# Performance work log

Measured on AMD Instinct MI355X. Metric: run time of the kernel, lower is better.

## Reference

```python
import jax, jax.numpy as jnp
import numpy as np

N_NODES = 50000
N_EDGES = 1600000
D_IN = 512
D_HEAD = 64
N_HEADS_L1 = 4


def _segment_mean(data, seg_ids, num_segments, counts):
    s = jax.ops.segment_sum(data, seg_ids, num_segments=num_segments)
    denom = jnp.maximum(counts, 1.0)
    return jnp.where(counts[:, None] > 0, s / denom[:, None], 0.0)


def setup_inputs() -> dict:
    key = jax.random.key(0)
    k1, k2, k3, k4 = jax.random.split(key, 4)
    node_features = jax.random.normal(k1, (N_NODES, D_IN), dtype=jnp.float32)
    edge_index = jax.random.randint(k2, (2, N_EDGES), 0, N_NODES, dtype=jnp.int32)
    W1 = jax.random.normal(k3, (N_HEADS_L1, D_IN, D_HEAD), dtype=jnp.float32) * (1.0 / np.sqrt(D_IN))
    W2 = jax.random.normal(k4, (N_HEADS_L1 * D_HEAD, D_HEAD), dtype=jnp.float32) * (1.0 / np.sqrt(N_HEADS_L1 * D_HEAD))
    return {"node_features": node_features, "edge_index": edge_index, "W1": W1, "W2": W2}


def reference(node_features, edge_index, W1, W2):
    n = node_features.shape[0]
    src = edge_index[0]  # segment ids (destination of aggregation in TF code)
    dst = edge_index[1]  # gathered neighbors
    counts = jax.ops.segment_sum(jnp.ones_like(src, dtype=node_features.dtype), src, num_segments=n)

    # Layer 1: 4 heads, Dense(64, no bias) -> gather(dst) -> unsorted_segment_mean(src) -> concat -> elu
    head_outs = []
    for i in range(N_HEADS_L1):
        t = node_features @ W1[i]                 # (N, 64)
        agg = _segment_mean(t[dst], src, n, counts)  # (N, 64)
        head_outs.append(agg)
    h = jax.nn.elu(jnp.concatenate(head_outs, axis=-1))  # (N, 256)

    # Layer 2: 1 head, linear activation
    t2 = h @ W2                                   # (N, 64)
    out = _segment_mean(t2[dst], src, n, counts)  # (N, 64)
    return out
```

## Files before the change

### kernel.cpp

```cpp
#include <hip/hip_runtime.h>
#include <hip/hip_bf16.h>
#include <stdint.h>

#define N_NODES 50000
#define N_EDGES 1600000
#define D_IN    512
#define D_H1    256
#define D_OUT   64

#define NBUK    196
#define MAXB    9216
#define EPB     4096
#define NPB     391
#define SLOT    96

typedef __attribute__((ext_vector_type(8))) short  short8;
typedef __attribute__((ext_vector_type(4))) float  f32x4;
typedef __attribute__((ext_vector_type(4))) unsigned int u32x4;
typedef __attribute__((ext_vector_type(2))) unsigned int u32x2;

static __device__ __forceinline__ unsigned short f2bf(float f) {
    union { float f; unsigned int u; } c; c.f = f;
    unsigned int u = c.u;
    return (unsigned short)((u + 0x7FFFu + ((u >> 16) & 1u)) >> 16);
}
static __device__ __forceinline__ float bf2f(unsigned short b) {
    union { unsigned int u; float f; } c; c.u = ((unsigned int)b) << 16;
    return c.f;
}
static __device__ __forceinline__ float bflo(unsigned int v) { return bf2f((unsigned short)(v & 0xffffu)); }
static __device__ __forceinline__ float bfhi(unsigned int v) { return bf2f((unsigned short)(v >> 16)); }


__global__ __launch_bounds__(256) void part_kernel(const int* __restrict__ src,
                                                   const int* __restrict__ dst,
                                                   int* __restrict__ gcnt,
                                                   unsigned int* __restrict__ gbuk) {
    __shared__ int hist[NBUK];
    __shared__ int lofs[NBUK];
    __shared__ int gbase[NBUK];
    __shared__ int sbuf[256];
    __shared__ unsigned int sorted[EPB];
    __shared__ unsigned char bid[EPB];

    const int t  = threadIdx.x;
    const int e0 = blockIdx.x * EPB;
    int ec = N_EDGES - e0; if (ec > EPB) ec = EPB;

    for (int i = t; i < NBUK; i += 256) hist[i] = 0;
    __syncthreads();

    unsigned int rec[16];
    int bb[16], idx[16];
#pragma unroll
    for (int j = 0; j < 16; ++j) {
        int i = j * 256 + t;
        if (i < ec) {
            int s = src[e0 + i], d = dst[e0 + i];
            int b = s >> 8;
            rec[j] = ((unsigned int)(s & 255) << 16) | (unsigned int)d;
            bb[j]  = b;
            idx[j] = atomicAdd(&hist[b], 1);
        } else bb[j] = -1;
    }
    __syncthreads();

    int v = (t < NBUK) ? hist[t] : 0;
    sbuf[t] = v;
    __syncthreads();
#pragma unroll
    for (int off = 1; off < 256; off <<= 1) {
        int x = (t >= off) ? sbuf[t - off] : 0;
        __syncthreads();
        sbuf[t] += x;
        __syncthreads();
    }
    if (t < NBUK) {
        lofs[t]  = sbuf[t] - v;
        gbase[t] = atomicAdd(&gcnt[t], v);
    }
    __syncthreads();

#pragma unroll
    for (int j = 0; j < 16; ++j) {
        if (bb[j] >= 0) {
            int p = lofs[bb[j]] + idx[j];
            sorted[p] = rec[j];
            bid[p] = (unsigned char)bb[j];
        }
    }
    __syncthreads();

    for (int i = t; i < ec; i += 256) {
        int b = bid[i];
        int p = gbase[b] + (i - lofs[b]);
        gbuk[(size_t)b * MAXB + p] = sorted[i];
    }
}


__global__ __launch_bounds__(256) void sort_kernel(const int* __restrict__ gcnt,
                                                   const unsigned int* __restrict__ gbuk,
                                                   unsigned short* __restrict__ sdst,
                                                   int* __restrict__ deg) {
    __shared__ int hist[256];
    __shared__ int nofs[256];
    __shared__ int sbuf[256];
    __shared__ unsigned short list[MAXB];

    const int t = threadIdx.x;
    const int b = blockIdx.x;
    const int cnt = gcnt[b];
    const unsigned int* buk = gbuk + (size_t)b * MAXB;

    hist[t] = 0;
    __syncthreads();
    for (int i = t; i < cnt; i += 256)
        atomicAdd(&hist[buk[i] >> 16], 1);
    __syncthreads();

    int v = hist[t];
    sbuf[t] = v;
    __syncthreads();
#pragma unroll
    for (int off = 1; off < 256; off <<= 1) {
        int x = (t >= off) ? sbuf[t - off] : 0;
        __syncthreads();
        sbuf[t] += x;
        __syncthreads();
    }
    nofs[t] = sbuf[t] - v;
    const int n = b * 256 + t;
    if (n < N_NODES) deg[n] = v;
    __syncthreads();

    for (int i = t; i < cnt; i += 256) {
        unsigned int r = buk[i];
        int p = atomicAdd(&nofs[r >> 16], 1);
        list[p] = (unsigned short)(r & 0xffffu);
    }
    __syncthreads();

    if (n < N_NODES && v > 0) {
        int beg = nofs[t] - v;
        unsigned short* out = sdst + (size_t)n * SLOT;
        for (int j = 0; j < v; ++j) out[j] = list[beg + j];
    }
}


__global__ void convw_kernel(const float* __restrict__ W1, const float* __restrict__ W2,
                             unsigned short* __restrict__ Bt1, unsigned short* __restrict__ Bt2) {
    int i = blockIdx.x * 256 + threadIdx.x;
    if (i < 4 * 512 * 64) {
        int h = i >> 15;
        int k = (i >> 6) & 511;
        int j = i & 63;
        Bt1[(h * 64 + j) * 512 + k] = f2bf(W1[i]);
    } else {
        int r = i - 4 * 512 * 64;
        if (r < 256 * 64) {
            int k = r >> 6;
            int n = r & 63;
            Bt2[n * 256 + k] = f2bf(W2[r]);
        }
    }
}


__global__ __launch_bounds__(512) void gemm1_kernel(const float* __restrict__ A,
                                                    const unsigned short* __restrict__ Bt,
                                                    unsigned short* __restrict__ C) {
    constexpr int BM = 128, BN = 256, BK = 32, LDK = 40, K = D_IN, M = N_NODES, N = D_H1;
    __shared__ unsigned short As[BM * LDK];
    __shared__ unsigned short Bs[BN * LDK];

    const int tid  = threadIdx.x;
    const int lane = tid & 63;
    const int w    = tid >> 6;
    const int wm   = (w >> 2) * 64;
    const int wn   = (w & 3) * 64;
    const int quad = lane >> 4;
    const int l15  = lane & 15;
    const int bm   = blockIdx.x;

    f32x4 acc[4][4];
#pragma unroll
    for (int mi = 0; mi < 4; ++mi)
#pragma unroll
        for (int ni = 0; ni < 4; ++ni)
            acc[mi][ni] = (f32x4){0.f, 0.f, 0.f, 0.f};

    const int r0 = tid >> 2;
    const int f8 = tid & 3;

    for (int k0 = 0; k0 < K; k0 += BK) {
        {
            int grow = bm * BM + r0;
            if (grow >= M) grow = M - 1;
            const float* ap = A + (size_t)grow * K + k0 + f8 * 8;
            f32x4 v0 = *(const f32x4*)ap;
            f32x4 v1 = *(const f32x4*)(ap + 4);
            u32x4 pk;
            pk[0] = (unsigned int)f2bf(v0[0]) | ((unsigned int)f2bf(v0[1]) << 16);
            pk[1] = (unsigned int)f2bf(v0[2]) | ((unsigned int)f2bf(v0[3]) << 16);
            pk[2] = (unsigned int)f2bf(v1[0]) | ((unsigned int)f2bf(v1[1]) << 16);
            pk[3] = (unsigned int)f2bf(v1[2]) | ((unsigned int)f2bf(v1[3]) << 16);
            *(u32x4*)&As[r0 * LDK + f8 * 8] = pk;
        }
        {
#pragma unroll
            for (int p = 0; p < 2; ++p) {
                int row = p * 128 + r0;
                u32x4 v = *(const u32x4*)(Bt + (size_t)row * K + k0 + f8 * 8);
                *(u32x4*)&Bs[row * LDK + f8 * 8] = v;
            }
        }
        __syncthreads();

        short8 af[4], bfr[4];
#pragma unroll
        for (int mi = 0; mi < 4; ++mi)
            af[mi] = *(const short8*)&As[(wm + mi * 16 + l15) * LDK + quad * 8];
#pragma unroll
        for (int ni = 0; ni < 4; ++ni)
            bfr[ni] = *(const short8*)&Bs[(wn + ni * 16 + l15) * LDK + quad * 8];
#pragma unroll
        for (int mi = 0; mi < 4; ++mi)
#pragma unroll
            for (int ni = 0; ni < 4; ++ni)
                acc[mi][ni] = __builtin_amdgcn_mfma_f32_16x16x32_bf16(af[mi], bfr[ni], acc[mi][ni], 0, 0, 0);
        __syncthreads();
    }

#pragma unroll
    for (int mi = 0; mi < 4; ++mi) {
        int row0 = bm * BM + wm + mi * 16 + quad * 4;
#pragma unroll
        for (int ni = 0; ni < 4; ++ni) {
            int col = wn + ni * 16 + l15;
#pragma unroll
            for (int r = 0; r < 4; ++r) {
                int row = row0 + r;
                if (row < M) C[(size_t)row * N + col] = f2bf(acc[mi][ni][r]);
            }
        }
    }
}


__global__ __launch_bounds__(256) void gemm2_kernel(const unsigned short* __restrict__ A,
                                                    const unsigned short* __restrict__ Bt,
                                                    unsigned short* __restrict__ C) {
    constexpr int BM = 64, BN = 64, BK = 32, LDK = 40, K = D_H1, M = N_NODES, N = D_OUT;
    __shared__ unsigned short As[BM * LDK];
    __shared__ unsigned short Bs[BN * LDK];

    const int tid  = threadIdx.x;
    const int lane = tid & 63;
    const int w    = tid >> 6;
    const int wm   = (w >> 1) * 32;
    const int wn   = (w & 1) * 32;
    const int quad = lane >> 4;
    const int l15  = lane & 15;
    const int bm   = blockIdx.x;

    f32x4 acc[2][2];
#pragma unroll
    for (int mi = 0; mi < 2; ++mi)
#pragma unroll
        for (int ni = 0; ni < 2; ++ni)
            acc[mi][ni] = (f32x4){0.f, 0.f, 0.f, 0.f};

    for (int k0 = 0; k0 < K; k0 += BK) {
        {
            int f8 = tid & 3;
            int r0 = tid >> 2;
            int grow = bm * BM + r0;
            if (grow >= M) grow = M - 1;
            u32x4 v = *(const u32x4*)(A + (size_t)grow * K + k0 + f8 * 8);
            *(u32x4*)&As[r0 * LDK + f8 * 8] = v;
        }
        {
            int f8 = tid & 3;
            int r0 = tid >> 2;
            u32x4 v = *(const u32x4*)(Bt + (size_t)r0 * K + k0 + f8 * 8);
            *(u32x4*)&Bs[r0 * LDK + f8 * 8] = v;
        }
        __syncthreads();

        short8 af[2], bfr[2];
#pragma unroll
        for (int mi = 0; mi < 2; ++mi)
            af[mi] = *(const short8*)&As[(wm + mi * 16 + l15) * LDK + quad * 8];
#pragma unroll
        for (int ni = 0; ni < 2; ++ni)
            bfr[ni] = *(const short8*)&Bs[(wn + ni * 16 + l15) * LDK + quad * 8];
#pragma unroll
        for (int mi = 0; mi < 2; ++mi)
#pragma unroll
            for (int ni = 0; ni < 2; ++ni)
                acc[mi][ni] = __builtin_amdgcn_mfma_f32_16x16x32_bf16(af[mi], bfr[ni], acc[mi][ni], 0, 0, 0);
        __syncthreads();
    }

#pragma unroll
    for (int mi = 0; mi < 2; ++mi) {
        int row0 = bm * BM + wm + mi * 16 + quad * 4;
#pragma unroll
        for (int ni = 0; ni < 2; ++ni) {
            int col = wn + ni * 16 + l15;
#pragma unroll
            for (int r = 0; r < 4; ++r) {
                int row = row0 + r;
                if (row < M) C[(size_t)row * N + col] = f2bf(acc[mi][ni][r]);
            }
        }
    }
}


__global__ __launch_bounds__(256) void agg1_kernel(const unsigned short* __restrict__ t,
                                                   const int* __restrict__ deg,
                                                   const unsigned short* __restrict__ sdst,
                                                   unsigned short* __restrict__ h) {
    int s = __builtin_amdgcn_readfirstlane(blockIdx.x * 4 + (threadIdx.x >> 6));
    int lane = threadIdx.x & 63;
    int sub = lane >> 5;
    int c   = lane & 31;
    int end = deg[s];
    const unsigned short* el = sdst + (size_t)s * SLOT;
    const unsigned short* base = t + 8 * c;

    float a[8];
#pragma unroll
    for (int k = 0; k < 8; ++k) a[k] = 0.f;

    int e = 0;
    for (; e + 8 <= end; e += 8) {
        int i0 = el[e + 0 + sub], i1 = el[e + 2 + sub];
        int i2 = el[e + 4 + sub], i3 = el[e + 6 + sub];
        u32x4 v0 = *(const u32x4*)(base + (size_t)i0 * D_H1);
        u32x4 v1 = *(const u32x4*)(base + (size_t)i1 * D_H1);
        u32x4 v2 = *(const u32x4*)(base + (size_t)i2 * D_H1);
        u32x4 v3 = *(const u32x4*)(base + (size_t)i3 * D_H1);
#pragma unroll
        for (int q = 0; q < 4; ++q) {
            a[2 * q]     += (bflo(v0[q]) + bflo(v1[q])) + (bflo(v2[q]) + bflo(v3[q]));
            a[2 * q + 1] += (bfhi(v0[q]) + bfhi(v1[q])) + (bfhi(v2[q]) + bfhi(v3[q]));
        }
    }
    for (; e + 2 <= end; e += 2) {
        int i0 = el[e + sub];
        u32x4 v = *(const u32x4*)(base + (size_t)i0 * D_H1);
#pragma unroll
        for (int q = 0; q < 4; ++q) {
            a[2 * q]     += bflo(v[q]);
            a[2 * q + 1] += bfhi(v[q]);
        }
    }
    if (e < end && sub == 0) {
        int i0 = el[e];
        u32x4 v = *(const u32x4*)(base + (size_t)i0 * D_H1);
#pragma unroll
        for (int q = 0; q < 4; ++q) {
            a[2 * q]     += bflo(v[q]);
            a[2 * q + 1] += bfhi(v[q]);
        }
    }
#pragma unroll
    for (int k = 0; k < 8; ++k) a[k] += __shfl_xor(a[k], 32);

    if (sub == 0) {
        float iv = (end > 0) ? (1.0f / (float)end) : 0.f;
        u32x4 pk;
#pragma unroll
        for (int q = 0; q < 4; ++q) {
            float m0 = a[2 * q] * iv, m1 = a[2 * q + 1] * iv;
            m0 = (m0 > 0.f) ? m0 : (__expf(m0) - 1.f);
            m1 = (m1 > 0.f) ? m1 : (__expf(m1) - 1.f);
            pk[q] = (unsigned int)f2bf(m0) | ((unsigned int)f2bf(m1) << 16);
        }
        *(u32x4*)&h[(size_t)s * D_H1 + 8 * c] = pk;
    }
}

__global__ __launch_bounds__(256) void agg2_kernel(const unsigned short* __restrict__ t2,
                                                   const int* __restrict__ deg,
                                                   const unsigned short* __restrict__ sdst,
                                                   float* __restrict__ out) {
    int s = __builtin_amdgcn_readfirstlane(blockIdx.x * 4 + (threadIdx.x >> 6));
    int lane = threadIdx.x & 63;
    int sub = lane >> 4;
    int c   = lane & 15;
    int end = deg[s];
    const unsigned short* el = sdst + (size_t)s * SLOT;
    const unsigned short* bb = t2 + 4 * c;

    float a0 = 0.f, a1 = 0.f, a2 = 0.f, a3 = 0.f;
    int e = 0;
    for (; e + 8 <= end; e += 8) {
        int i0 = el[e + sub], i1 = el[e + 4 + sub];
        u32x2 v0 = *(const u32x2*)(bb + (size_t)i0 * D_OUT);
        u32x2 v1 = *(const u32x2*)(bb + (size_t)i1 * D_OUT);
        a0 += bflo(v0[0]) + bflo(v1[0]);
        a1 += bfhi(v0[0]) + bfhi(v1[0]);
        a2 += bflo(v0[1]) + bflo(v1[1]);
        a3 += bfhi(v0[1]) + bfhi(v1[1]);
    }
    for (; e + 4 <= end; e += 4) {
        int i0 = el[e + sub];
        u32x2 v = *(const u32x2*)(bb + (size_t)i0 * D_OUT);
        a0 += bflo(v[0]); a1 += bfhi(v[0]); a2 += bflo(v[1]); a3 += bfhi(v[1]);
    }
    int rem = end - e;
    if (sub < rem) {
        int i0 = el[e + sub];
        u32x2 v = *(const u32x2*)(bb + (size_t)i0 * D_OUT);
        a0 += bflo(v[0]); a1 += bfhi(v[0]); a2 += bflo(v[1]); a3 += bfhi(v[1]);
    }
    a0 += __shfl_xor(a0, 16); a1 += __shfl_xor(a1, 16);
    a2 += __shfl_xor(a2, 16); a3 += __shfl_xor(a3, 16);
    a0 += __shfl_xor(a0, 32); a1 += __shfl_xor(a1, 32);
    a2 += __shfl_xor(a2, 32); a3 += __shfl_xor(a3, 32);
    if (sub == 0) {
        float iv = (end > 0) ? (1.0f / (float)end) : 0.f;
        f32x4 r; r[0] = a0 * iv; r[1] = a1 * iv; r[2] = a2 * iv; r[3] = a3 * iv;
        *(f32x4*)(out + (size_t)s * D_OUT + 4 * c) = r;
    }
}


extern "C" void kernel_launch(void* const* d_in, const int* in_sizes, int n_in,
                              void* d_out, int out_size, void* d_ws, size_t ws_size,
                              hipStream_t stream) {
    const float* X  = (const float*)d_in[0];
    const int*   ei = (const int*)d_in[1];
    const float* W1 = (const float*)d_in[2];
    const float* W2 = (const float*)d_in[3];
    const int* src = ei;
    const int* dst = ei + N_EDGES;

    char* ws = (char*)d_ws;
    size_t off = 0;
    auto alloc = [&](size_t bytes) {
        off = (off + 255) & ~(size_t)255;
        void* p = ws + off;
        off += bytes;
        return p;
    };
    int*          gcnt = (int*)alloc((size_t)NBUK * 4);
    unsigned int* gbuk = (unsigned int*)alloc((size_t)NBUK * MAXB * 4);
    unsigned short* sdst = (unsigned short*)alloc(((size_t)N_NODES * SLOT + 64) * 2);
    int*          deg  = (int*)alloc((size_t)N_NODES * 4);
    unsigned short* Bt1 = (unsigned short*)alloc((size_t)D_H1 * D_IN * 2);
    unsigned short* Bt2 = (unsigned short*)alloc((size_t)D_OUT * D_H1 * 2);
    unsigned short* t1  = (unsigned short*)alloc((size_t)N_NODES * D_H1 * 2);
    unsigned short* h   = (unsigned short*)alloc((size_t)N_NODES * D_H1 * 2);
    unsigned short* t2  = (unsigned short*)alloc((size_t)N_NODES * D_OUT * 2);

    hipMemsetAsync(gcnt, 0, (size_t)NBUK * 4, stream);

    part_kernel<<<NPB, 256, 0, stream>>>(src, dst, gcnt, gbuk);
    sort_kernel<<<NBUK, 256, 0, stream>>>(gcnt, gbuk, sdst, deg);
    convw_kernel<<<(4 * 512 * 64 + 256 * 64 + 255) / 256, 256, 0, stream>>>(W1, W2, Bt1, Bt2);

    gemm1_kernel<<<(N_NODES + 127) / 128, 512, 0, stream>>>(X, Bt1, t1);
    agg1_kernel<<<N_NODES / 4, 256, 0, stream>>>(t1, deg, sdst, h);
    gemm2_kernel<<<(N_NODES + 63) / 64, 256, 0, stream>>>(h, Bt2, t2);
    agg2_kernel<<<N_NODES / 4, 256, 0, stream>>>(t2, deg, sdst, (float*)d_out);
}
```

Baseline: 361.1 us.

## Sort neighbor lists and sweep gathers in synchronized row bands for cache locality

The sort kernel now insertion-sorts each node's neighbor list so gathered row indices ascend. agg1 is restructured so each half-wave owns 7 nodes and walks their neighbor lists in 25 index bands of 2048 rows, with a block barrier after each band. All resident waves then touch the same slice of t1 at the same time, so gathers should hit L2/MALL instead of DRAM. The cost is a serial insertion sort per node, a lower-parallelism grid of 896 blocks with scalar per-edge loops and divergent while-loops, and 25 barriers per block.

```diff
diff --git a/kernel.cpp b/kernel.cpp
--- a/kernel.cpp
+++ b/kernel.cpp
@@ -13,6 +13,10 @@
 #define EPB     4096
 #define NPB     391
 #define SLOT    96
+
+#define AGB     896
+#define NSN     7
+#define RR      25
 
 typedef __attribute__((ext_vector_type(8))) short  short8;
 typedef __attribute__((ext_vector_type(4))) float  f32x4;
@@ -141,8 +145,17 @@
     }
     __syncthreads();
 
+    const int endp = nofs[t];
+    const int beg  = endp - v;
+    for (int j = beg + 1; j < endp; ++j) {
+        unsigned short key = list[j];
+        int k = j - 1;
+        while (k >= beg && list[k] > key) { list[k + 1] = list[k]; --k; }
+        list[k + 1] = key;
+    }
+    __syncthreads();
+
     if (n < N_NODES && v > 0) {
-        int beg = nofs[t] - v;
         unsigned short* out = sdst + (size_t)n * SLOT;
         for (int j = 0; j < v; ++j) out[j] = list[beg + j];
     }
@@ -320,70 +333,69 @@
 }
 
 
-__global__ __launch_bounds__(256) void agg1_kernel(const unsigned short* __restrict__ t,
-                                                   const int* __restrict__ deg,
-                                                   const unsigned short* __restrict__ sdst,
-                                                   unsigned short* __restrict__ h) {
-    int s = __builtin_amdgcn_readfirstlane(blockIdx.x * 4 + (threadIdx.x >> 6));
-    int lane = threadIdx.x & 63;
-    int sub = lane >> 5;
-    int c   = lane & 31;
-    int end = deg[s];
-    const unsigned short* el = sdst + (size_t)s * SLOT;
+__global__ __launch_bounds__(256, 4) void agg1_kernel(const unsigned short* __restrict__ t,
+                                                      const int* __restrict__ deg,
+                                                      const unsigned short* __restrict__ sdst,
+                                                      unsigned short* __restrict__ h) {
+    const int w    = threadIdx.x >> 6;
+    const int lane = threadIdx.x & 63;
+    const int hs   = lane >> 5;
+    const int c    = lane & 31;
+    const int half_id = (blockIdx.x * 4 + w) * 2 + hs;
+    const int s0 = half_id * NSN;
     const unsigned short* base = t + 8 * c;
 
-    float a[8];
-#pragma unroll
-    for (int k = 0; k < 8; ++k) a[k] = 0.f;
-
-    int e = 0;
-    for (; e + 8 <= end; e += 8) {
-        int i0 = el[e + 0 + sub], i1 = el[e + 2 + sub];
-        int i2 = el[e + 4 + sub], i3 = el[e + 6 + sub];
-        u32x4 v0 = *(const u32x4*)(base + (size_t)i0 * D_H1);
-        u32x4 v1 = *(const u32x4*)(base + (size_t)i1 * D_H1);
-        u32x4 v2 = *(const u32x4*)(base + (size_t)i2 * D_H1);
-        u32x4 v3 = *(const u32x4*)(base + (size_t)i3 * D_H1);
-#pragma unroll
-        for (int q = 0; q < 4; ++q) {
-            a[2 * q]     += (bflo(v0[q]) + bflo(v1[q])) + (bflo(v2[q]) + bflo(v3[q]));
-            a[2 * q + 1] += (bfhi(v0[q]) + bfhi(v1[q])) + (bfhi(v2[q]) + bfhi(v3[q]));
-        }
-    }
-    for (; e + 2 <= end; e += 2) {
-        int i0 = el[e + sub];
-        u32x4 v = *(const u32x4*)(base + (size_t)i0 * D_H1);
-#pragma unroll
-        for (int q = 0; q < 4; ++q) {
-            a[2 * q]     += bflo(v[q]);
-            a[2 * q + 1] += bfhi(v[q]);
-        }
-    }
-    if (e < end && sub == 0) {
-        int i0 = el[e];
-        u32x4 v = *(const u32x4*)(base + (size_t)i0 * D_H1);
-#pragma unroll
-        for (int q = 0; q < 4; ++q) {
-            a[2 * q]     += bflo(v[q]);
-            a[2 * q + 1] += bfhi(v[q]);
-        }
-    }
-#pragma unroll
-    for (int k = 0; k < 8; ++k) a[k] += __shfl_xor(a[k], 32);
-
-    if (sub == 0) {
-        float iv = (end > 0) ? (1.0f / (float)end) : 0.f;
-        u32x4 pk;
-#pragma unroll
-        for (int q = 0; q < 4; ++q) {
-            float m0 = a[2 * q] * iv, m1 = a[2 * q + 1] * iv;
-            m0 = (m0 > 0.f) ? m0 : (__expf(m0) - 1.f);
-            m1 = (m1 > 0.f) ? m1 : (__expf(m1) - 1.f);
-            pk[q] = (unsigned int)f2bf(m0) | ((unsigned int)f2bf(m1) << 16);
-        }
-        *(u32x4*)&h[(size_t)s * D_H1 + 8 * c] = pk;
-    }
-}
+    float acc[NSN][8];
+    int   cur[NSN], dg[NSN];
+#pragma unroll
+    for (int i = 0; i < NSN; ++i) {
+        int s = s0 + i;
+        dg[i] = (s < N_NODES) ? deg[s] : 0;
+        cur[i] = 0;
+#pragma unroll
+        for (int k = 0; k < 8; ++k) acc[i][k] = 0.f;
+    }
+
+    for (int r = 0; r < RR; ++r) {
+        const int hi = (r == RR - 1) ? 65536 : ((r + 1) << 11);
+#pragma unroll
+        for (int i = 0; i < NSN; ++i) {
+            const unsigned short* el = sdst + (size_t)(s0 + i) * SLOT;
+            int e = cur[i];
+            const int d = dg[i];
+            while (e < d) {
+                int idx = el[e];
+                if (idx >= hi) break;
+                u32x4 v = *(const u32x4*)(base + (size_t)idx * D_H1);
+                acc[i][0] += bflo(v[0]); acc[i][1] += bfhi(v[0]);
+                acc[i][2] += bflo(v[1]); acc[i][3] += bfhi(v[1]);
+                acc[i][4] += bflo(v[2]); acc[i][5] += bfhi(v[2]);
+                acc[i][6] += bflo(v[3]); acc[i][7] += bfhi(v[3]);
+                ++e;
+            }
+            cur[i] = e;
+        }
+        __syncthreads();
+    }
+
+#pragma unroll
+    for (int i = 0; i < NSN; ++i) {
+        int s = s0 + i;
+        if (s < N_NODES) {
+            float iv = (dg[i] > 0) ? (1.0f / (float)dg[i]) : 0.f;
+            u32x4 pk;
+#pragma unroll
+            for (int q = 0; q < 4; ++q) {
+                float m0 = acc[i][2 * q] * iv, m1 = acc[i][2 * q + 1] * iv;
+                m0 = (m0 > 0.f) ? m0 : (__expf(m0) - 1.f);
+                m1 = (m1 > 0.f) ? m1 : (__expf(m1) - 1.f);
+                pk[q] = (unsigned int)f2bf(m0) | ((unsigned int)f2bf(m1) << 16);
+            }
+            *(u32x4*)&h[(size_t)s * D_H1 + 8 * c] = pk;
+        }
+    }
+}
+
 
 __global__ __launch_bounds__(256) void agg2_kernel(const unsigned short* __restrict__ t2,
                                                    const int* __restrict__ deg,
@@ -451,7 +463,7 @@
     };
     int*          gcnt = (int*)alloc((size_t)NBUK * 4);
     unsigned int* gbuk = (unsigned int*)alloc((size_t)NBUK * MAXB * 4);
-    unsigned short* sdst = (unsigned short*)alloc(((size_t)N_NODES * SLOT + 64) * 2);
+    unsigned short* sdst = (unsigned short*)alloc(((size_t)(N_NODES + NSN * 16) * SLOT) * 2);
     int*          deg  = (int*)alloc((size_t)N_NODES * 4);
     unsigned short* Bt1 = (unsigned short*)alloc((size_t)D_H1 * D_IN * 2);
     unsigned short* Bt2 = (unsigned short*)alloc((size_t)D_OUT * D_H1 * 2);
@@ -466,7 +478,7 @@
     convw_kernel<<<(4 * 512 * 64 + 256 * 64 + 255) / 256, 256, 0, stream>>>(W1, W2, Bt1, Bt2);
 
     gemm1_kernel<<<(N_NODES + 127) / 128, 512, 0, stream>>>(X, Bt1, t1);
-    agg1_kernel<<<N_NODES / 4, 256, 0, stream>>>(t1, deg, sdst, h);
+    agg1_kernel<<<AGB, 256, 0, stream>>>(t1, deg, sdst, h);
     gemm2_kernel<<<(N_NODES + 63) / 64, 256, 0, stream>>>(h, Bt2, t2);
     agg2_kernel<<<N_NODES / 4, 256, 0, stream>>>(t2, deg, sdst, (float*)d_out);
 }
```

Result: slower. 668.2 us (+85.1%).

## Bin neighbor lists by source-row range and sync waves per range in agg1

Applied to the files above, without the earlier changes.

The sort kernel now builds a 16-way sub-histogram per node, keyed on the high bits of the gathered neighbor index. Each neighbor list therefore comes out ordered by row range of t1, and per-range counts go into a new cnt16 buffer. agg1 walks the 13 ranges in order and places a block barrier after each one, so the four waves of a block gather from the same region of t1 together, aiming for better cache hit rates. The cost is a larger shared histogram, extra global writes for the counts, a barrier per range, and less unrolling in the gather loop (4 edges per step instead of 8). Blocks across the GPU are not kept in step, so the gain in locality may be limited.

```diff
diff --git a/kernel.cpp b/kernel.cpp
--- a/kernel.cpp
+++ b/kernel.cpp
@@ -13,6 +13,9 @@
 #define EPB     4096
 #define NPB     391
 #define SLOT    96
+
+#define RSH     12
+#define RR      13
 
 typedef __attribute__((ext_vector_type(8))) short  short8;
 typedef __attribute__((ext_vector_type(4))) float  f32x4;
@@ -102,9 +105,10 @@
 __global__ __launch_bounds__(256) void sort_kernel(const int* __restrict__ gcnt,
                                                    const unsigned int* __restrict__ gbuk,
                                                    unsigned short* __restrict__ sdst,
-                                                   int* __restrict__ deg) {
-    __shared__ int hist[256];
-    __shared__ int nofs[256];
+                                                   int* __restrict__ deg,
+                                                   unsigned short* __restrict__ cnt16) {
+    __shared__ int hist2[256 * 16];
+    __shared__ int nbase[256];
     __shared__ int sbuf[256];
     __shared__ unsigned short list[MAXB];
 
@@ -113,14 +117,23 @@
     const int cnt = gcnt[b];
     const unsigned int* buk = gbuk + (size_t)b * MAXB;
 
-    hist[t] = 0;
-    __syncthreads();
-    for (int i = t; i < cnt; i += 256)
-        atomicAdd(&hist[buk[i] >> 16], 1);
-    __syncthreads();
-
-    int v = hist[t];
-    sbuf[t] = v;
+#pragma unroll
+    for (int j = 0; j < 16; ++j) hist2[j * 256 + t] = 0;
+    __syncthreads();
+
+    for (int i = t; i < cnt; i += 256) {
+        unsigned int r = buk[i];
+        int key2 = (int)((r >> 16) << 4) | (int)((r & 0xffffu) >> RSH);
+        atomicAdd(&hist2[key2], 1);
+    }
+    __syncthreads();
+
+    int cr[16];
+    int tot = 0;
+#pragma unroll
+    for (int r = 0; r < 16; ++r) { cr[r] = hist2[t * 16 + r]; tot += cr[r]; }
+
+    sbuf[t] = tot;
     __syncthreads();
 #pragma unroll
     for (int off = 1; off < 256; off <<= 1) {
@@ -129,22 +142,38 @@
         sbuf[t] += x;
         __syncthreads();
     }
-    nofs[t] = sbuf[t] - v;
+    int base = sbuf[t] - tot;
+    nbase[t] = base;
+
     const int n = b * 256 + t;
-    if (n < N_NODES) deg[n] = v;
+    {
+        int run = base;
+#pragma unroll
+        for (int r = 0; r < 16; ++r) {
+            hist2[t * 16 + r] = run;
+            run += cr[r];
+        }
+    }
+    if (n < N_NODES) {
+        deg[n] = tot;
+        unsigned short* cp = cnt16 + (size_t)n * 16;
+#pragma unroll
+        for (int r = 0; r < 16; ++r) cp[r] = (unsigned short)cr[r];
+    }
     __syncthreads();
 
     for (int i = t; i < cnt; i += 256) {
         unsigned int r = buk[i];
-        int p = atomicAdd(&nofs[r >> 16], 1);
+        int key2 = (int)((r >> 16) << 4) | (int)((r & 0xffffu) >> RSH);
+        int p = atomicAdd(&hist2[key2], 1);
         list[p] = (unsigned short)(r & 0xffffu);
     }
     __syncthreads();
 
-    if (n < N_NODES && v > 0) {
-        int beg = nofs[t] - v;
+    if (n < N_NODES && tot > 0) {
+        int beg = nbase[t];
         unsigned short* out = sdst + (size_t)n * SLOT;
-        for (int j = 0; j < v; ++j) out[j] = list[beg + j];
+        for (int j = 0; j < tot; ++j) out[j] = list[beg + j];
     }
 }
 
@@ -321,58 +350,66 @@
 
 
 __global__ __launch_bounds__(256) void agg1_kernel(const unsigned short* __restrict__ t,
+                                                   const unsigned short* __restrict__ cnt16,
+                                                   const unsigned short* __restrict__ sdst,
                                                    const int* __restrict__ deg,
-                                                   const unsigned short* __restrict__ sdst,
                                                    unsigned short* __restrict__ h) {
     int s = __builtin_amdgcn_readfirstlane(blockIdx.x * 4 + (threadIdx.x >> 6));
     int lane = threadIdx.x & 63;
     int sub = lane >> 5;
     int c   = lane & 31;
-    int end = deg[s];
     const unsigned short* el = sdst + (size_t)s * SLOT;
     const unsigned short* base = t + 8 * c;
+    const unsigned short* cp = cnt16 + (size_t)s * 16;
 
     float a[8];
 #pragma unroll
     for (int k = 0; k < 8; ++k) a[k] = 0.f;
 
     int e = 0;
-    for (; e + 8 <= end; e += 8) {
-        int i0 = el[e + 0 + sub], i1 = el[e + 2 + sub];
-        int i2 = el[e + 4 + sub], i3 = el[e + 6 + sub];
-        u32x4 v0 = *(const u32x4*)(base + (size_t)i0 * D_H1);
-        u32x4 v1 = *(const u32x4*)(base + (size_t)i1 * D_H1);
-        u32x4 v2 = *(const u32x4*)(base + (size_t)i2 * D_H1);
-        u32x4 v3 = *(const u32x4*)(base + (size_t)i3 * D_H1);
-#pragma unroll
-        for (int q = 0; q < 4; ++q) {
-            a[2 * q]     += (bflo(v0[q]) + bflo(v1[q])) + (bflo(v2[q]) + bflo(v3[q]));
-            a[2 * q + 1] += (bfhi(v0[q]) + bfhi(v1[q])) + (bfhi(v2[q]) + bfhi(v3[q]));
-        }
-    }
-    for (; e + 2 <= end; e += 2) {
-        int i0 = el[e + sub];
-        u32x4 v = *(const u32x4*)(base + (size_t)i0 * D_H1);
-#pragma unroll
-        for (int q = 0; q < 4; ++q) {
-            a[2 * q]     += bflo(v[q]);
-            a[2 * q + 1] += bfhi(v[q]);
-        }
-    }
-    if (e < end && sub == 0) {
-        int i0 = el[e];
-        u32x4 v = *(const u32x4*)(base + (size_t)i0 * D_H1);
-#pragma unroll
-        for (int q = 0; q < 4; ++q) {
-            a[2 * q]     += bflo(v[q]);
-            a[2 * q + 1] += bfhi(v[q]);
-        }
-    }
+    for (int r = 0; r < RR; ++r) {
+        int e_end = e + cp[r];
+        for (; e + 4 <= e_end; e += 4) {
+            int i0 = el[e + sub], i1 = el[e + 2 + sub];
+            u32x4 v0 = *(const u32x4*)(base + (size_t)i0 * D_H1);
+            u32x4 v1 = *(const u32x4*)(base + (size_t)i1 * D_H1);
+#pragma unroll
+            for (int q = 0; q < 4; ++q) {
+                a[2 * q]     += bflo(v0[q]) + bflo(v1[q]);
+                a[2 * q + 1] += bfhi(v0[q]) + bfhi(v1[q]);
+            }
+        }
+        if (e + 2 <= e_end) {
+            int i0 = el[e + sub];
+            u32x4 v = *(const u32x4*)(base + (size_t)i0 * D_H1);
+#pragma unroll
+            for (int q = 0; q < 4; ++q) {
+                a[2 * q]     += bflo(v[q]);
+                a[2 * q + 1] += bfhi(v[q]);
+            }
+            e += 2;
+        }
+        if (e < e_end) {
+            if (sub == 0) {
+                int i0 = el[e];
+                u32x4 v = *(const u32x4*)(base + (size_t)i0 * D_H1);
+#pragma unroll
+                for (int q = 0; q < 4; ++q) {
+                    a[2 * q]     += bflo(v[q]);
+                    a[2 * q + 1] += bfhi(v[q]);
+                }
+            }
+            e = e_end;
+        }
+        __syncthreads();
+    }
+
 #pragma unroll
     for (int k = 0; k < 8; ++k) a[k] += __shfl_xor(a[k], 32);
 
     if (sub == 0) {
-        float iv = (end > 0) ? (1.0f / (float)end) : 0.f;
+        int dg = deg[s];
+        float iv = (dg > 0) ? (1.0f / (float)dg) : 0.f;
         u32x4 pk;
 #pragma unroll
         for (int q = 0; q < 4; ++q) {
@@ -384,6 +421,7 @@
         *(u32x4*)&h[(size_t)s * D_H1 + 8 * c] = pk;
     }
 }
+
 
 __global__ __launch_bounds__(256) void agg2_kernel(const unsigned short* __restrict__ t2,
                                                    const int* __restrict__ deg,
@@ -453,6 +491,7 @@
     unsigned int* gbuk = (unsigned int*)alloc((size_t)NBUK * MAXB * 4);
     unsigned short* sdst = (unsigned short*)alloc(((size_t)N_NODES * SLOT + 64) * 2);
     int*          deg  = (int*)alloc((size_t)N_NODES * 4);
+    unsigned short* cnt16 = (unsigned short*)alloc((size_t)N_NODES * 16 * 2);
     unsigned short* Bt1 = (unsigned short*)alloc((size_t)D_H1 * D_IN * 2);
     unsigned short* Bt2 = (unsigned short*)alloc((size_t)D_OUT * D_H1 * 2);
     unsigned short* t1  = (unsigned short*)alloc((size_t)N_NODES * D_H1 * 2);
@@ -462,11 +501,11 @@
     hipMemsetAsync(gcnt, 0, (size_t)NBUK * 4, stream);
 
     part_kernel<<<NPB, 256, 0, stream>>>(src, dst, gcnt, gbuk);
-    sort_kernel<<<NBUK, 256, 0, stream>>>(gcnt, gbuk, sdst, deg);
+    sort_kernel<<<NBUK, 256, 0, stream>>>(gcnt, gbuk, sdst, deg, cnt16);
     convw_kernel<<<(4 * 512 * 64 + 256 * 64 + 255) / 256, 256, 0, stream>>>(W1, W2, Bt1, Bt2);
 
     gemm1_kernel<<<(N_NODES + 127) / 128, 512, 0, stream>>>(X, Bt1, t1);
-    agg1_kernel<<<N_NODES / 4, 256, 0, stream>>>(t1, deg, sdst, h);
+    agg1_kernel<<<N_NODES / 4, 256, 0, stream>>>(t1, cnt16, sdst, deg, h);
     gemm2_kernel<<<(N_NODES + 63) / 64, 256, 0, stream>>>(h, Bt2, t2);
     agg2_kernel<<<N_NODES / 4, 256, 0, stream>>>(t2, deg, sdst, (float*)d_out);
 }
```

After: 414.5 us. +14.8%, slower.
